# Kernel optimization log

Hardware: AMD Instinct MI355X
Metric: run time of the kernel (lower is better)

The kernel has to match this reference:

```python
import jax, jax.numpy as jnp
import numpy as np

K = 1  # Op(k=1): num = num_op // k == num_op, so random.sample selects ALL ops (deterministic)


def setup_inputs() -> dict:
    key = jax.random.key(0)
    k1, k2, k3, k4, k5 = jax.random.split(key, 5)
    N, D = 50000, 128
    NUM_OP, E = 8, 400000
    return {
        "x": jax.random.normal(k1, (N, D), dtype=jnp.float32),
        "edge_vals": jax.random.uniform(k2, (NUM_OP, E), dtype=jnp.float32),
        "ws": jax.random.uniform(k3, (NUM_OP,), dtype=jnp.float32),
        "edge_rows": jax.random.randint(k4, (NUM_OP, E), 0, N, dtype=jnp.int32),
        "edge_cols": jax.random.randint(k5, (NUM_OP, E), 0, N, dtype=jnp.int32),
    }


def reference(x, edge_vals, ws, edge_rows, edge_cols):
    # out = (1/num) * sum_i ws[i] * spmm(A_i, x), with num = num_op (k=1 -> all ops sampled)
    N = x.shape[0]
    num_op = ws.shape[0]
    num = num_op // K
    out = jnp.zeros_like(x)
    for i in range(num_op):  # small fixed set of ops (NAS mixture), not a data dim
        msg = edge_vals[i][:, None] * x[edge_cols[i]]  # [E, D] gather + scale
        out = out + ws[i] * jax.ops.segment_sum(msg, edge_rows[i], num_segments=N)
    return out / num
```

## Files before the change

kernel.cpp:

```cpp
#include <hip/hip_runtime.h>
#include <hip/hip_fp16.h>


#define D_DIM 128
#define RPB_SHIFT 5
#define RPB 32
#define CSEG 4
#define CSEG_SHIFT 14
#define NB (RPB * CSEG)
#define MAXB 2048
#define CHUNK 8192
#define SCAN_BLOCK 1024
#define CVT_BLOCKS 1024
#define CNT_BLOCKS 256

typedef unsigned long long ull;

static __device__ __forceinline__ unsigned short f2bf(float f) {
    unsigned int u = __float_as_uint(f);
    u += 0x7FFFu + ((u >> 16) & 1u);
    return (unsigned short)(u >> 16);
}

static __device__ __forceinline__ unsigned short f2h(float f) {
    return __half_as_ushort(__float2half(f));
}

static __device__ __forceinline__ ull pack2f(float a, float b) {
    return (ull)__float_as_uint(a) | ((ull)__float_as_uint(b) << 32);
}

__global__ __launch_bounds__(256) void spmm_scatter_kernel(
    const float* __restrict__ x, const float* __restrict__ edge_vals,
    const float* __restrict__ ws, const int* __restrict__ edge_rows,
    const int* __restrict__ edge_cols, float* __restrict__ out,
    int E, float inv_num)
{
    const int  op   = blockIdx.y;
    const long base = (long)op * (long)E;
    const float wscale = ws[op] * inv_num;
    const int lane = threadIdx.x & 63;
    const int wave = blockIdx.x * (blockDim.x >> 6) + (threadIdx.x >> 6);
    const int nwaves = gridDim.x * (blockDim.x >> 6);
    for (int e = wave; e < E; e += nwaves) {
        const int row = edge_rows[base + e];
        const int col = edge_cols[base + e];
        const float v = edge_vals[base + e] * wscale;
        const float2 xv = *reinterpret_cast<const float2*>(x + (long)col * D_DIM + lane * 2);
        float* o = out + (long)row * D_DIM + lane * 2;
        atomicAdd(o, xv.x * v);
        atomicAdd(o + 1, xv.y * v);
    }
}

__global__ __launch_bounds__(256) void convert_count_kernel(
    const float4* __restrict__ x4, ull* __restrict__ xh, int n4,
    const int* __restrict__ rows, int* __restrict__ gcount, long n, int B)
{
    __shared__ int h[MAXB];
    if (blockIdx.x < CVT_BLOCKS) {
        const int stride = CVT_BLOCKS * 256;
        for (int i = blockIdx.x * 256 + threadIdx.x; i < n4; i += stride) {
            const float4 v = x4[i];
            const ull p =
                (ull)f2h(v.x)
                | ((ull)f2h(v.y) << 16)
                | ((ull)f2h(v.z) << 32)
                | ((ull)f2h(v.w) << 48);
            xh[i] = p;
        }
    } else {
        const int cb = blockIdx.x - CVT_BLOCKS;
        for (int i = threadIdx.x; i < B; i += 256) h[i] = 0;
        __syncthreads();
        const long n4r = n >> 2;
        for (long q = (long)cb * 256 + threadIdx.x; q < n4r;
             q += (long)CNT_BLOCKS * 256) {
            const int4 r = reinterpret_cast<const int4*>(rows)[q];
            atomicAdd(&h[r.x >> RPB_SHIFT], 1);
            atomicAdd(&h[r.y >> RPB_SHIFT], 1);
            atomicAdd(&h[r.z >> RPB_SHIFT], 1);
            atomicAdd(&h[r.w >> RPB_SHIFT], 1);
        }
        if (cb == 0 && (long)threadIdx.x < (n & 3))
            atomicAdd(&h[rows[(n4r << 2) + threadIdx.x] >> RPB_SHIFT], 1);
        __syncthreads();
        for (int i = threadIdx.x; i < B; i += 256)
            if (h[i]) atomicAdd(&gcount[i], h[i]);
    }
}

__global__ __launch_bounds__(SCAN_BLOCK) void scan_kernel(
    int* __restrict__ cursors, int* __restrict__ offsets, int N)
{
    __shared__ int sdata[SCAN_BLOCK];
    __shared__ int carry_s;
    if (threadIdx.x == 0) carry_s = 0;
    __syncthreads();
    for (int base = 0; base < N; base += SCAN_BLOCK) {
        const int i = base + (int)threadIdx.x;
        const int v = (i < N) ? cursors[i] : 0;
        sdata[threadIdx.x] = v;
        __syncthreads();
        for (int ofs = 1; ofs < SCAN_BLOCK; ofs <<= 1) {
            int t = (threadIdx.x >= (unsigned)ofs) ? sdata[threadIdx.x - ofs] : 0;
            __syncthreads();
            sdata[threadIdx.x] += t;
            __syncthreads();
        }
        const int incl  = sdata[threadIdx.x];
        const int carry = carry_s;
        if (i < N) {
            const int excl = carry + incl - v;
            offsets[i] = excl;
            cursors[i] = excl;
        }
        __syncthreads();
        if (threadIdx.x == SCAN_BLOCK - 1) carry_s = carry + incl;
        __syncthreads();
    }
    if (threadIdx.x == 0) offsets[N] = carry_s;
}

__global__ __launch_bounds__(1024, 8) void scatter_bucket_kernel(
    const int* __restrict__ edge_rows, const int* __restrict__ edge_cols,
    const float* __restrict__ edge_vals, const float* __restrict__ ws,
    int* __restrict__ gcursor, ull* __restrict__ records,
    int E, float inv_num, int B)
{
    __shared__ int hist[MAXB];
    const int  op   = blockIdx.y;
    const long base = (long)op * (long)E;
    const int  e0   = blockIdx.x * CHUNK;
    const int  e1   = min(e0 + CHUNK, E);
    const float wscale = ws[op] * inv_num;
    const int  tid  = (int)threadIdx.x;
    const int*   erow = edge_rows + base;
    const int*   ecol = edge_cols + base;
    const float* eval = edge_vals + base;

    for (int i = tid; i < B; i += 1024) hist[i] = 0;
    __syncthreads();

    const int gA = e0 + tid * 4;
    const int gB = gA + 4096;
    int4 rA = make_int4(0, 0, 0, 0), rB = make_int4(0, 0, 0, 0);
    int  mA = 0, mB = 0;

    { const int rem = e1 - gA;
      if (rem >= 4) { rA = *reinterpret_cast<const int4*>(erow + gA); mA = 4; }
      else if (rem > 0) { mA = rem; rA.x = erow[gA];
          if (rem > 1) rA.y = erow[gA + 1];
          if (rem > 2) rA.z = erow[gA + 2]; } }
    { const int rem = e1 - gB;
      if (rem >= 4) { rB = *reinterpret_cast<const int4*>(erow + gB); mB = 4; }
      else if (rem > 0) { mB = rem; rB.x = erow[gB];
          if (rem > 1) rB.y = erow[gB + 1];
          if (rem > 2) rB.z = erow[gB + 2]; } }

    if (mA > 0) atomicAdd(&hist[rA.x >> RPB_SHIFT], 1);
    if (mA > 1) atomicAdd(&hist[rA.y >> RPB_SHIFT], 1);
    if (mA > 2) atomicAdd(&hist[rA.z >> RPB_SHIFT], 1);
    if (mA > 3) atomicAdd(&hist[rA.w >> RPB_SHIFT], 1);
    if (mB > 0) atomicAdd(&hist[rB.x >> RPB_SHIFT], 1);
    if (mB > 1) atomicAdd(&hist[rB.y >> RPB_SHIFT], 1);
    if (mB > 2) atomicAdd(&hist[rB.z >> RPB_SHIFT], 1);
    if (mB > 3) atomicAdd(&hist[rB.w >> RPB_SHIFT], 1);
    __syncthreads();

    for (int i = tid; i < B; i += 1024) {
        const int c = hist[i];
        hist[i] = c ? atomicAdd(&gcursor[i], c) : 0;
    }
    __syncthreads();

#define EMIT(RW, CW, VW)                                                       \
    { const int bin_ = (RW) >> RPB_SHIFT;                                      \
      const int pos_ = atomicAdd(&hist[bin_], 1);                              \
      const ull rec_ = ((ull)__float_as_uint((VW) * wscale) << 32)             \
          | ((unsigned int)((RW) & (RPB - 1)) << 16) | (unsigned int)(CW);     \
      records[pos_] = rec_; }

    if (mA > 0) {
        int4 c = make_int4(0, 0, 0, 0); float4 v = make_float4(0.f, 0.f, 0.f, 0.f);
        if (mA == 4) { c = *reinterpret_cast<const int4*>(ecol + gA);
                       v = *reinterpret_cast<const float4*>(eval + gA); }
        else { c.x = ecol[gA]; v.x = eval[gA];
               if (mA > 1) { c.y = ecol[gA + 1]; v.y = eval[gA + 1]; }
               if (mA > 2) { c.z = ecol[gA + 2]; v.z = eval[gA + 2]; } }
        EMIT(rA.x, c.x, v.x)
        if (mA > 1) EMIT(rA.y, c.y, v.y)
        if (mA > 2) EMIT(rA.z, c.z, v.z)
        if (mA > 3) EMIT(rA.w, c.w, v.w)
    }
    if (mB > 0) {
        int4 c = make_int4(0, 0, 0, 0); float4 v = make_float4(0.f, 0.f, 0.f, 0.f);
        if (mB == 4) { c = *reinterpret_cast<const int4*>(ecol + gB);
                       v = *reinterpret_cast<const float4*>(eval + gB); }
        else { c.x = ecol[gB]; v.x = eval[gB];
               if (mB > 1) { c.y = ecol[gB + 1]; v.y = eval[gB + 1]; }
               if (mB > 2) { c.z = ecol[gB + 2]; v.z = eval[gB + 2]; } }
        EMIT(rB.x, c.x, v.x)
        if (mB > 1) EMIT(rB.y, c.y, v.y)
        if (mB > 2) EMIT(rB.z, c.z, v.z)
        if (mB > 3) EMIT(rB.w, c.w, v.w)
    }
#undef EMIT
}

__global__ __launch_bounds__(512) void sort_bucket_kernel(
    const ull* __restrict__ records, unsigned int* __restrict__ sorted32,
    const int* __restrict__ boff, int* __restrict__ binoff, int N, int B)
{
    __shared__ int h[NB];
    __shared__ int cur[NB];
    __shared__ int wsum[2];
    __shared__ int woff[2];
    const int bkt   = blockIdx.x;
    const int start = boff[bkt], end = boff[bkt + 1];
    const int tid   = (int)threadIdx.x;
    const int lane  = tid & 63;
    const int w     = tid >> 6;

    if (tid < NB) h[tid] = 0;
    __syncthreads();
    for (int i = start + tid; i < end; i += 512) {
        const unsigned int lo = (unsigned int)records[i];
        const int bin = (int)((lo >> 16) << 2) | (int)((lo & 0xFFFFu) >> CSEG_SHIFT);
        atomicAdd(&h[bin], 1);
    }
    __syncthreads();
    if (tid < NB) {
        const int v = h[tid];
        int incl = v;
        #pragma unroll
        for (int o = 1; o < 64; o <<= 1) {
            const int t = __shfl_up(incl, o);
            if (lane >= o) incl += t;
        }
        if (lane == 63) wsum[w] = incl;
        __syncthreads();
        if (tid == 0) { woff[0] = 0; woff[1] = wsum[0]; }
        __syncthreads();
        const int excl = start + woff[w] + incl - v;
        cur[tid] = excl;
        binoff[bkt * NB + tid] = excl;
    } else {
        __syncthreads();
        __syncthreads();
    }
    if (tid == 0 && bkt == B - 1) binoff[B * NB] = end;
    __syncthreads();
    for (int i = start + tid; i < end; i += 512) {
        const ull r = records[i];
        const unsigned int lo = (unsigned int)r;
        const int bin = (int)((lo >> 16) << 2) | (int)((lo & 0xFFFFu) >> CSEG_SHIFT);
        const int pos = atomicAdd(&cur[bin], 1);
        sorted32[pos] = (lo & 0xFFFFu)
            | ((unsigned int)f2bf(__uint_as_float((unsigned int)(r >> 32))) << 16);
    }
}

#define GREC(RK)                                                               \
    { const unsigned int p_ = *reinterpret_cast<const unsigned int*>(          \
          xh + (size_t)((RK)&0xFFFFu) * D_DIM + lane * 2);                     \
      const float v_ = __uint_as_float((RK)&0xFFFF0000u);                      \
      const __half2 h2_ = *reinterpret_cast<const __half2*>(&p_);              \
      ax += v_ * __half2float(h2_.x);                                          \
      ay += v_ * __half2float(h2_.y); }

__global__ __launch_bounds__(256) void gather_seg_kernel(
    const unsigned short* __restrict__ xh, const int* __restrict__ binoff,
    const unsigned int* __restrict__ sorted32, float* __restrict__ out,
    int N, int B)
{
    const int tid  = (int)threadIdx.x;
    const int lane = tid & 63;
    const int w    = tid >> 6;
    const int bkt  = blockIdx.x;
    const int rl0  = w * 8;
    const int bb   = bkt * NB + rl0 * CSEG;

    float accx[8], accy[8];
    int jcur[8];
    #pragma unroll
    for (int rr = 0; rr < 8; ++rr) {
        accx[rr] = 0.f; accy[rr] = 0.f;
        jcur[rr] = __builtin_amdgcn_readfirstlane(binoff[bb + rr * CSEG]);
    }

    for (int seg = 0; seg < CSEG; ++seg) {
        int jend[8];
        #pragma unroll
        for (int rr = 0; rr < 8; ++rr)
            jend[rr] = __builtin_amdgcn_readfirstlane(
                binoff[bb + rr * CSEG + seg + 1]);
        #pragma unroll
        for (int rr = 0; rr < 8; ++rr) {
            int j = jcur[rr];
            const int je = jend[rr];
            float ax = accx[rr], ay = accy[rr];
            for (; j + 15 < je; j += 16) {
                const unsigned int r0  = sorted32[j];
                const unsigned int r1  = sorted32[j + 1];
                const unsigned int r2  = sorted32[j + 2];
                const unsigned int r3  = sorted32[j + 3];
                const unsigned int r4  = sorted32[j + 4];
                const unsigned int r5  = sorted32[j + 5];
                const unsigned int r6  = sorted32[j + 6];
                const unsigned int r7  = sorted32[j + 7];
                const unsigned int r8  = sorted32[j + 8];
                const unsigned int r9  = sorted32[j + 9];
                const unsigned int r10 = sorted32[j + 10];
                const unsigned int r11 = sorted32[j + 11];
                const unsigned int r12 = sorted32[j + 12];
                const unsigned int r13 = sorted32[j + 13];
                const unsigned int r14 = sorted32[j + 14];
                const unsigned int r15 = sorted32[j + 15];
                GREC(r0)  GREC(r1)  GREC(r2)  GREC(r3)
                GREC(r4)  GREC(r5)  GREC(r6)  GREC(r7)
                GREC(r8)  GREC(r9)  GREC(r10) GREC(r11)
                GREC(r12) GREC(r13) GREC(r14) GREC(r15)
            }
            if (j + 7 < je) {
                const unsigned int r0 = sorted32[j];
                const unsigned int r1 = sorted32[j + 1];
                const unsigned int r2 = sorted32[j + 2];
                const unsigned int r3 = sorted32[j + 3];
                const unsigned int r4 = sorted32[j + 4];
                const unsigned int r5 = sorted32[j + 5];
                const unsigned int r6 = sorted32[j + 6];
                const unsigned int r7 = sorted32[j + 7];
                GREC(r0) GREC(r1) GREC(r2) GREC(r3)
                GREC(r4) GREC(r5) GREC(r6) GREC(r7)
                j += 8;
            }
            if (j + 3 < je) {
                const unsigned int r0 = sorted32[j];
                const unsigned int r1 = sorted32[j + 1];
                const unsigned int r2 = sorted32[j + 2];
                const unsigned int r3 = sorted32[j + 3];
                GREC(r0) GREC(r1) GREC(r2) GREC(r3)
                j += 4;
            }
            if (j + 1 < je) {
                const unsigned int r0 = sorted32[j];
                const unsigned int r1 = sorted32[j + 1];
                GREC(r0) GREC(r1)
                j += 2;
            }
            if (j < je) {
                const unsigned int r0 = sorted32[j];
                GREC(r0)
            }
            accx[rr] = ax; accy[rr] = ay;
            jcur[rr] = je;
        }
    }

    const int row0 = (bkt << RPB_SHIFT) + rl0;
    #pragma unroll
    for (int rr = 0; rr < 8; ++rr) {
        const int row = row0 + rr;
        if (row < N)
            __builtin_nontemporal_store(pack2f(accx[rr], accy[rr]),
                reinterpret_cast<ull*>(out + (size_t)row * D_DIM + lane * 2));
    }
}

__global__ __launch_bounds__(1024) void gather_filter2_kernel(
    const unsigned short* __restrict__ xh, const int* __restrict__ boff,
    const ull* __restrict__ records, float* __restrict__ out, int N)
{
    const int lane = threadIdx.x & 63;
    const int wv   = threadIdx.x >> 6;
    const int bkt  = blockIdx.x;
    const int row0 = (bkt << RPB_SHIFT) + wv * 2;
    const int row1 = row0 + 1;
    const int start = boff[bkt], end = boff[bkt + 1];

    float a0x = 0.f, a0y = 0.f, a1x = 0.f, a1y = 0.f;
    for (int c = start; c < end; c += 64) {
        const int idx = c + lane;
        unsigned int lo = 0xFFFF0000u, hi = 0;
        if (idx < end) {
            const ull r = __builtin_nontemporal_load(&records[idx]);
            lo = (unsigned int)r;
            hi = (unsigned int)(r >> 32);
        }
        ull mask = __ballot((lo >> 17) == (unsigned int)wv);
        while (mask) {
            const int j = __ffsll(mask) - 1;
            mask &= mask - 1;
            const unsigned int lj = __shfl(lo, j);
            const float v = __uint_as_float(__shfl(hi, j));
            const unsigned int col = lj & 0xFFFFu;
            const unsigned int p = *reinterpret_cast<const unsigned int*>(
                xh + (size_t)col * D_DIM + lane * 2);
            const __half2 h2 = *reinterpret_cast<const __half2*>(&p);
            const float px = __half2float(h2.x);
            const float py = __half2float(h2.y);
            if (lj & 0x10000u) { a1x += v * px; a1y += v * py; }
            else               { a0x += v * px; a0y += v * py; }
        }
    }
    if (row0 < N)
        __builtin_nontemporal_store(pack2f(a0x, a0y),
            reinterpret_cast<ull*>(out + (size_t)row0 * D_DIM + lane * 2));
    if (row1 < N)
        __builtin_nontemporal_store(pack2f(a1x, a1y),
            reinterpret_cast<ull*>(out + (size_t)row1 * D_DIM + lane * 2));
}

extern "C" void kernel_launch(void* const* d_in, const int* in_sizes, int n_in,
                              void* d_out, int out_size, void* d_ws, size_t ws_size,
                              hipStream_t stream)
{
    const float* x         = (const float*)d_in[0];
    const float* edge_vals = (const float*)d_in[1];
    const float* ws        = (const float*)d_in[2];
    const int*   edge_rows = (const int*)d_in[3];
    const int*   edge_cols = (const int*)d_in[4];
    float*       out       = (float*)d_out;

    const int num_op = in_sizes[2];
    const int E      = in_sizes[1] / num_op;
    const int N      = in_sizes[0] / D_DIM;
    const long Etot  = (long)num_op * (long)E;
    const int  B     = (N + RPB - 1) / RPB;
    const float inv_num = 1.0f / (float)num_op;

    const size_t off_boff    = 0;
    const size_t off_gcur    = ((size_t)(B + 1) * 4 + 255) & ~(size_t)255;
    const size_t off_binoff  = (off_gcur + (size_t)B * 4 + 255) & ~(size_t)255;
    const size_t off_xh      = (off_binoff + ((size_t)B * NB + 1) * 4 + 255) & ~(size_t)255;
    const size_t off_records = (off_xh + (size_t)N * D_DIM * 2 + 255) & ~(size_t)255;
    const size_t off_sorted  = off_records + (size_t)Etot * 8;
    const size_t need_sort   = off_sorted + (size_t)Etot * 4;
    const size_t need_filter = off_sorted;

    if (ws_size < need_filter || B > MAXB || N > 65535) {
        (void)hipMemsetAsync(d_out, 0, (size_t)out_size * sizeof(float), stream);
        dim3 grid(256, num_op, 1);
        spmm_scatter_kernel<<<grid, 256, 0, stream>>>(
            x, edge_vals, ws, edge_rows, edge_cols, out, E, inv_num);
        return;
    }

    int* boff    = (int*)((char*)d_ws + off_boff);
    int* gcursor = (int*)((char*)d_ws + off_gcur);
    int* binoff  = (int*)((char*)d_ws + off_binoff);
    unsigned short* xh = (unsigned short*)((char*)d_ws + off_xh);
    ull* records = (ull*)((char*)d_ws + off_records);
    unsigned int* sorted32 = (unsigned int*)((char*)d_ws + off_sorted);

    (void)hipMemsetAsync(gcursor, 0, (size_t)B * 4, stream);

    convert_count_kernel<<<CVT_BLOCKS + CNT_BLOCKS, 256, 0, stream>>>(
        (const float4*)x, (ull*)xh, N * D_DIM / 4, edge_rows, gcursor, Etot, B);
    scan_kernel<<<1, SCAN_BLOCK, 0, stream>>>(gcursor, boff, B);

    dim3 sgrid((E + CHUNK - 1) / CHUNK, num_op, 1);
    scatter_bucket_kernel<<<sgrid, 1024, 0, stream>>>(
        edge_rows, edge_cols, edge_vals, ws, gcursor, records, E, inv_num, B);

    if (ws_size >= need_sort) {
        sort_bucket_kernel<<<B, 512, 0, stream>>>(
            records, sorted32, boff, binoff, N, B);
        gather_seg_kernel<<<B, 256, 0, stream>>>(
            xh, binoff, sorted32, out, N, B);
    } else {
        gather_filter2_kernel<<<B, 1024, 0, stream>>>(xh, boff, records, out, N);
    }
}
```

Before: 157.6 us.

## Fuse per-bucket sort and gather into one kernel using LDS record buffer

Merges the bucket sort kernel and the segmented gather kernel into a single kernel that counting-sorts each bucket's records into shared memory and then gathers directly from LDS. This removes the global sorted32 array write and reread, the binoff array, and one kernel launch. Buckets larger than the LDS capacity fall back to a ballot-filter gather over the raw records. Each block now uses 512 threads with 4 rows per wave and about 17KB of LDS, which may reduce occupancy.

```diff
diff --git a/kernel.cpp b/kernel.cpp
--- a/kernel.cpp
+++ b/kernel.cpp
@@ -8,6 +8,7 @@
 #define CSEG 4
 #define CSEG_SHIFT 14
 #define NB (RPB * CSEG)
+#define LREC_CAP 4096
 #define MAXB 2048
 #define CHUNK 8192
 #define SCAN_BLOCK 1024
@@ -208,59 +209,6 @@
 #undef EMIT
 }
 
-__global__ __launch_bounds__(512) void sort_bucket_kernel(
-    const ull* __restrict__ records, unsigned int* __restrict__ sorted32,
-    const int* __restrict__ boff, int* __restrict__ binoff, int N, int B)
-{
-    __shared__ int h[NB];
-    __shared__ int cur[NB];
-    __shared__ int wsum[2];
-    __shared__ int woff[2];
-    const int bkt   = blockIdx.x;
-    const int start = boff[bkt], end = boff[bkt + 1];
-    const int tid   = (int)threadIdx.x;
-    const int lane  = tid & 63;
-    const int w     = tid >> 6;
-
-    if (tid < NB) h[tid] = 0;
-    __syncthreads();
-    for (int i = start + tid; i < end; i += 512) {
-        const unsigned int lo = (unsigned int)records[i];
-        const int bin = (int)((lo >> 16) << 2) | (int)((lo & 0xFFFFu) >> CSEG_SHIFT);
-        atomicAdd(&h[bin], 1);
-    }
-    __syncthreads();
-    if (tid < NB) {
-        const int v = h[tid];
-        int incl = v;
-        #pragma unroll
-        for (int o = 1; o < 64; o <<= 1) {
-            const int t = __shfl_up(incl, o);
-            if (lane >= o) incl += t;
-        }
-        if (lane == 63) wsum[w] = incl;
-        __syncthreads();
-        if (tid == 0) { woff[0] = 0; woff[1] = wsum[0]; }
-        __syncthreads();
-        const int excl = start + woff[w] + incl - v;
-        cur[tid] = excl;
-        binoff[bkt * NB + tid] = excl;
-    } else {
-        __syncthreads();
-        __syncthreads();
-    }
-    if (tid == 0 && bkt == B - 1) binoff[B * NB] = end;
-    __syncthreads();
-    for (int i = start + tid; i < end; i += 512) {
-        const ull r = records[i];
-        const unsigned int lo = (unsigned int)r;
-        const int bin = (int)((lo >> 16) << 2) | (int)((lo & 0xFFFFu) >> CSEG_SHIFT);
-        const int pos = atomicAdd(&cur[bin], 1);
-        sorted32[pos] = (lo & 0xFFFFu)
-            | ((unsigned int)f2bf(__uint_as_float((unsigned int)(r >> 32))) << 16);
-    }
-}
-
 #define GREC(RK)                                                               \
     { const unsigned int p_ = *reinterpret_cast<const unsigned int*>(          \
           xh + (size_t)((RK)&0xFFFFu) * D_DIM + lane * 2);                     \
@@ -269,147 +217,172 @@
       ax += v_ * __half2float(h2_.x);                                          \
       ay += v_ * __half2float(h2_.y); }
 
-__global__ __launch_bounds__(256) void gather_seg_kernel(
-    const unsigned short* __restrict__ xh, const int* __restrict__ binoff,
-    const unsigned int* __restrict__ sorted32, float* __restrict__ out,
-    int N, int B)
-{
+__global__ __launch_bounds__(512) void sortgather_kernel(
+    const unsigned short* __restrict__ xh, const int* __restrict__ boff,
+    const ull* __restrict__ records, float* __restrict__ out, int N, int B)
+{
+    __shared__ int h[NB];
+    __shared__ int cur[NB];
+    __shared__ int boffL[NB + 1];
+    __shared__ int wsum[2];
+    __shared__ int woff[2];
+    __shared__ unsigned int lrec[LREC_CAP];
+
     const int tid  = (int)threadIdx.x;
     const int lane = tid & 63;
     const int w    = tid >> 6;
     const int bkt  = blockIdx.x;
-    const int rl0  = w * 8;
-    const int bb   = bkt * NB + rl0 * CSEG;
-
-    float accx[8], accy[8];
-    int jcur[8];
+    const int start = boff[bkt], end = boff[bkt + 1];
+    const int len   = end - start;
+    const int rl0   = w * 4;
+
+    float accx[4], accy[4];
     #pragma unroll
-    for (int rr = 0; rr < 8; ++rr) {
-        accx[rr] = 0.f; accy[rr] = 0.f;
-        jcur[rr] = __builtin_amdgcn_readfirstlane(binoff[bb + rr * CSEG]);
-    }
-
-    for (int seg = 0; seg < CSEG; ++seg) {
-        int jend[8];
-        #pragma unroll
-        for (int rr = 0; rr < 8; ++rr)
-            jend[rr] = __builtin_amdgcn_readfirstlane(
-                binoff[bb + rr * CSEG + seg + 1]);
-        #pragma unroll
-        for (int rr = 0; rr < 8; ++rr) {
-            int j = jcur[rr];
-            const int je = jend[rr];
-            float ax = accx[rr], ay = accy[rr];
-            for (; j + 15 < je; j += 16) {
-                const unsigned int r0  = sorted32[j];
-                const unsigned int r1  = sorted32[j + 1];
-                const unsigned int r2  = sorted32[j + 2];
-                const unsigned int r3  = sorted32[j + 3];
-                const unsigned int r4  = sorted32[j + 4];
-                const unsigned int r5  = sorted32[j + 5];
-                const unsigned int r6  = sorted32[j + 6];
-                const unsigned int r7  = sorted32[j + 7];
-                const unsigned int r8  = sorted32[j + 8];
-                const unsigned int r9  = sorted32[j + 9];
-                const unsigned int r10 = sorted32[j + 10];
-                const unsigned int r11 = sorted32[j + 11];
-                const unsigned int r12 = sorted32[j + 12];
-                const unsigned int r13 = sorted32[j + 13];
-                const unsigned int r14 = sorted32[j + 14];
-                const unsigned int r15 = sorted32[j + 15];
-                GREC(r0)  GREC(r1)  GREC(r2)  GREC(r3)
-                GREC(r4)  GREC(r5)  GREC(r6)  GREC(r7)
-                GREC(r8)  GREC(r9)  GREC(r10) GREC(r11)
-                GREC(r12) GREC(r13) GREC(r14) GREC(r15)
+    for (int q = 0; q < 4; ++q) { accx[q] = 0.f; accy[q] = 0.f; }
+
+    if (len > LREC_CAP) {
+        for (int c = start; c < end; c += 64) {
+            const int idx = c + lane;
+            unsigned int lo = 0xFFFFFFFFu, hi = 0;
+            if (idx < end) {
+                const ull r = records[idx];
+                lo = (unsigned int)r;
+                hi = (unsigned int)(r >> 32);
             }
-            if (j + 7 < je) {
-                const unsigned int r0 = sorted32[j];
-                const unsigned int r1 = sorted32[j + 1];
-                const unsigned int r2 = sorted32[j + 2];
-                const unsigned int r3 = sorted32[j + 3];
-                const unsigned int r4 = sorted32[j + 4];
-                const unsigned int r5 = sorted32[j + 5];
-                const unsigned int r6 = sorted32[j + 6];
-                const unsigned int r7 = sorted32[j + 7];
-                GREC(r0) GREC(r1) GREC(r2) GREC(r3)
-                GREC(r4) GREC(r5) GREC(r6) GREC(r7)
-                j += 8;
+            const int rl = (int)((lo >> 16) & (RPB - 1));
+            ull mask = __ballot(idx < end && (rl >> 2) == w);
+            while (mask) {
+                const int jb = __ffsll(mask) - 1;
+                mask &= mask - 1;
+                const unsigned int lj = __shfl(lo, jb);
+                const float v = __uint_as_float(__shfl(hi, jb));
+                const unsigned int col = lj & 0xFFFFu;
+                const unsigned int p = *reinterpret_cast<const unsigned int*>(
+                    xh + (size_t)col * D_DIM + lane * 2);
+                const __half2 h2 = *reinterpret_cast<const __half2*>(&p);
+                const float px = __half2float(h2.x);
+                const float py = __half2float(h2.y);
+                const int q = (int)((lj >> 16) & 3u);
+                if      (q == 0) { accx[0] += v * px; accy[0] += v * py; }
+                else if (q == 1) { accx[1] += v * px; accy[1] += v * py; }
+                else if (q == 2) { accx[2] += v * px; accy[2] += v * py; }
+                else             { accx[3] += v * px; accy[3] += v * py; }
             }
-            if (j + 3 < je) {
-                const unsigned int r0 = sorted32[j];
-                const unsigned int r1 = sorted32[j + 1];
-                const unsigned int r2 = sorted32[j + 2];
-                const unsigned int r3 = sorted32[j + 3];
-                GREC(r0) GREC(r1) GREC(r2) GREC(r3)
-                j += 4;
+        }
+    } else {
+        if (tid < NB) h[tid] = 0;
+        __syncthreads();
+        for (int i = start + tid; i < end; i += 512) {
+            const unsigned int lo = (unsigned int)records[i];
+            const int bin = (int)((lo >> 16) << 2)
+                          | (int)((lo & 0xFFFFu) >> CSEG_SHIFT);
+            atomicAdd(&h[bin], 1);
+        }
+        __syncthreads();
+        if (tid < NB) {
+            const int v = h[tid];
+            int incl = v;
+            #pragma unroll
+            for (int o = 1; o < 64; o <<= 1) {
+                const int t = __shfl_up(incl, o);
+                if (lane >= o) incl += t;
             }
-            if (j + 1 < je) {
-                const unsigned int r0 = sorted32[j];
-                const unsigned int r1 = sorted32[j + 1];
-                GREC(r0) GREC(r1)
-                j += 2;
+            if (lane == 63) wsum[w] = incl;
+            __syncthreads();
+            if (tid == 0) { woff[0] = 0; woff[1] = wsum[0]; }
+            __syncthreads();
+            const int excl = woff[w] + incl - v;
+            cur[tid] = excl;
+            boffL[tid] = excl;
+        } else {
+            __syncthreads();
+            __syncthreads();
+        }
+        if (tid == 0) boffL[NB] = len;
+        __syncthreads();
+        for (int i = start + tid; i < end; i += 512) {
+            const ull r = records[i];
+            const unsigned int lo = (unsigned int)r;
+            const int bin = (int)((lo >> 16) << 2)
+                          | (int)((lo & 0xFFFFu) >> CSEG_SHIFT);
+            const int pos = atomicAdd(&cur[bin], 1);
+            lrec[pos] = (lo & 0xFFFFu)
+                | ((unsigned int)f2bf(__uint_as_float((unsigned int)(r >> 32))) << 16);
+        }
+        __syncthreads();
+        for (int seg = 0; seg < CSEG; ++seg) {
+            #pragma unroll
+            for (int q = 0; q < 4; ++q) {
+                const int bin = (rl0 + q) * CSEG + seg;
+                int j        = boffL[bin];
+                const int je = boffL[bin + 1];
+                float ax = accx[q], ay = accy[q];
+                for (; j + 15 < je; j += 16) {
+                    const unsigned int r0  = lrec[j];
+                    const unsigned int r1  = lrec[j + 1];
+                    const unsigned int r2  = lrec[j + 2];
+                    const unsigned int r3  = lrec[j + 3];
+                    const unsigned int r4  = lrec[j + 4];
+                    const unsigned int r5  = lrec[j + 5];
+                    const unsigned int r6  = lrec[j + 6];
+                    const unsigned int r7  = lrec[j + 7];
+                    const unsigned int r8  = lrec[j + 8];
+                    const unsigned int r9  = lrec[j + 9];
+                    const unsigned int r10 = lrec[j + 10];
+                    const unsigned int r11 = lrec[j + 11];
+                    const unsigned int r12 = lrec[j + 12];
+                    const unsigned int r13 = lrec[j + 13];
+                    const unsigned int r14 = lrec[j + 14];
+                    const unsigned int r15 = lrec[j + 15];
+                    GREC(r0)  GREC(r1)  GREC(r2)  GREC(r3)
+                    GREC(r4)  GREC(r5)  GREC(r6)  GREC(r7)
+                    GREC(r8)  GREC(r9)  GREC(r10) GREC(r11)
+                    GREC(r12) GREC(r13) GREC(r14) GREC(r15)
+                }
+                if (j + 7 < je) {
+                    const unsigned int r0 = lrec[j];
+                    const unsigned int r1 = lrec[j + 1];
+                    const unsigned int r2 = lrec[j + 2];
+                    const unsigned int r3 = lrec[j + 3];
+                    const unsigned int r4 = lrec[j + 4];
+                    const unsigned int r5 = lrec[j + 5];
+                    const unsigned int r6 = lrec[j + 6];
+                    const unsigned int r7 = lrec[j + 7];
+                    GREC(r0) GREC(r1) GREC(r2) GREC(r3)
+                    GREC(r4) GREC(r5) GREC(r6) GREC(r7)
+                    j += 8;
+                }
+                if (j + 3 < je) {
+                    const unsigned int r0 = lrec[j];
+                    const unsigned int r1 = lrec[j + 1];
+                    const unsigned int r2 = lrec[j + 2];
+                    const unsigned int r3 = lrec[j + 3];
+                    GREC(r0) GREC(r1) GREC(r2) GREC(r3)
+                    j += 4;
+                }
+                if (j + 1 < je) {
+                    const unsigned int r0 = lrec[j];
+                    const unsigned int r1 = lrec[j + 1];
+                    GREC(r0) GREC(r1)
+                    j += 2;
+                }
+                if (j < je) {
+                    const unsigned int r0 = lrec[j];
+                    GREC(r0)
+                }
+                accx[q] = ax; accy[q] = ay;
             }
-            if (j < je) {
-                const unsigned int r0 = sorted32[j];
-                GREC(r0)
-            }
-            accx[rr] = ax; accy[rr] = ay;
-            jcur[rr] = je;
         }
     }
 
     const int row0 = (bkt << RPB_SHIFT) + rl0;
     #pragma unroll
-    for (int rr = 0; rr < 8; ++rr) {
-        const int row = row0 + rr;
+    for (int q = 0; q < 4; ++q) {
+        const int row = row0 + q;
         if (row < N)
-            __builtin_nontemporal_store(pack2f(accx[rr], accy[rr]),
+            __builtin_nontemporal_store(pack2f(accx[q], accy[q]),
                 reinterpret_cast<ull*>(out + (size_t)row * D_DIM + lane * 2));
     }
-}
-
-__global__ __launch_bounds__(1024) void gather_filter2_kernel(
-    const unsigned short* __restrict__ xh, const int* __restrict__ boff,
-    const ull* __restrict__ records, float* __restrict__ out, int N)
-{
-    const int lane = threadIdx.x & 63;
-    const int wv   = threadIdx.x >> 6;
-    const int bkt  = blockIdx.x;
-    const int row0 = (bkt << RPB_SHIFT) + wv * 2;
-    const int row1 = row0 + 1;
-    const int start = boff[bkt], end = boff[bkt + 1];
-
-    float a0x = 0.f, a0y = 0.f, a1x = 0.f, a1y = 0.f;
-    for (int c = start; c < end; c += 64) {
-        const int idx = c + lane;
-        unsigned int lo = 0xFFFF0000u, hi = 0;
-        if (idx < end) {
-            const ull r = __builtin_nontemporal_load(&records[idx]);
-            lo = (unsigned int)r;
-            hi = (unsigned int)(r >> 32);
-        }
-        ull mask = __ballot((lo >> 17) == (unsigned int)wv);
-        while (mask) {
-            const int j = __ffsll(mask) - 1;
-            mask &= mask - 1;
-            const unsigned int lj = __shfl(lo, j);
-            const float v = __uint_as_float(__shfl(hi, j));
-            const unsigned int col = lj & 0xFFFFu;
-            const unsigned int p = *reinterpret_cast<const unsigned int*>(
-                xh + (size_t)col * D_DIM + lane * 2);
-            const __half2 h2 = *reinterpret_cast<const __half2*>(&p);
-            const float px = __half2float(h2.x);
-            const float py = __half2float(h2.y);
-            if (lj & 0x10000u) { a1x += v * px; a1y += v * py; }
-            else               { a0x += v * px; a0y += v * py; }
-        }
-    }
-    if (row0 < N)
-        __builtin_nontemporal_store(pack2f(a0x, a0y),
-            reinterpret_cast<ull*>(out + (size_t)row0 * D_DIM + lane * 2));
-    if (row1 < N)
-        __builtin_nontemporal_store(pack2f(a1x, a1y),
-            reinterpret_cast<ull*>(out + (size_t)row1 * D_DIM + lane * 2));
 }
 
 extern "C" void kernel_launch(void* const* d_in, const int* in_sizes, int n_in,
@@ -432,14 +405,11 @@
 
     const size_t off_boff    = 0;
     const size_t off_gcur    = ((size_t)(B + 1) * 4 + 255) & ~(size_t)255;
-    const size_t off_binoff  = (off_gcur + (size_t)B * 4 + 255) & ~(size_t)255;
-    const size_t off_xh      = (off_binoff + ((size_t)B * NB + 1) * 4 + 255) & ~(size_t)255;
+    const size_t off_xh      = (off_gcur + (size_t)B * 4 + 255) & ~(size_t)255;
     const size_t off_records = (off_xh + (size_t)N * D_DIM * 2 + 255) & ~(size_t)255;
-    const size_t off_sorted  = off_records + (size_t)Etot * 8;
-    const size_t need_sort   = off_sorted + (size_t)Etot * 4;
-    const size_t need_filter = off_sorted;
-
-    if (ws_size < need_filter || B > MAXB || N > 65535) {
+    const size_t need        = off_records + (size_t)Etot * 8;
+
+    if (ws_size < need || B > MAXB || N > 65535) {
         (void)hipMemsetAsync(d_out, 0, (size_t)out_size * sizeof(float), stream);
         dim3 grid(256, num_op, 1);
         spmm_scatter_kernel<<<grid, 256, 0, stream>>>(
@@ -449,10 +419,8 @@
 
     int* boff    = (int*)((char*)d_ws + off_boff);
     int* gcursor = (int*)((char*)d_ws + off_gcur);
-    int* binoff  = (int*)((char*)d_ws + off_binoff);
     unsigned short* xh = (unsigned short*)((char*)d_ws + off_xh);
     ull* records = (ull*)((char*)d_ws + off_records);
-    unsigned int* sorted32 = (unsigned int*)((char*)d_ws + off_sorted);
 
     (void)hipMemsetAsync(gcursor, 0, (size_t)B * 4, stream);
 
@@ -464,12 +432,5 @@
     scatter_bucket_kernel<<<sgrid, 1024, 0, stream>>>(
         edge_rows, edge_cols, edge_vals, ws, gcursor, records, E, inv_num, B);
 
-    if (ws_size >= need_sort) {
-        sort_bucket_kernel<<<B, 512, 0, stream>>>(
-            records, sorted32, boff, binoff, N, B);
-        gather_seg_kernel<<<B, 256, 0, stream>>>(
-            xh, binoff, sorted32, out, N, B);
-    } else {
-        gather_filter2_kernel<<<B, 1024, 0, stream>>>(xh, boff, records, out, N);
-    }
-}
+    sortgather_kernel<<<B, 512, 0, stream>>>(xh, boff, records, out, N, B);
+}
```

Measured after the change: 156.4 us (median of 2 runs). No clear change (-0.8%).
